# Optimization experiments

Measured on AMD Instinct MI355X. Metric: run time of the kernel, lower is better.

The kernel has to match this reference:

```python
import jax, jax.numpy as jnp
import numpy as np
import math

B, S, D = 1, 4096, 512
H, KVH, DH = 8, 4, 64
DH2 = DH // 2
M = int(math.isqrt(S))           # product-key grid side, S == M*M
K = 8                            # top_k
ROPE_BASE = 10000.0


def rope_cos_sin(seq_len, dh, base):
    inv_freq = 1.0 / (base ** (jnp.arange(0, dh, 2, dtype=jnp.float32) / dh))
    t = jnp.arange(seq_len, dtype=jnp.float32)
    freqs = jnp.outer(t, inv_freq)                      # (S, dh/2)
    emb = jnp.concatenate([freqs, freqs], axis=-1)      # (S, dh)
    return jnp.cos(emb), jnp.sin(emb)


def apply_rope(x, cos, sin):
    # x: (B, H, S, dh); half-split rotation (llama-style)
    dh2 = x.shape[-1] // 2
    rot = jnp.concatenate([-x[..., dh2:], x[..., :dh2]], axis=-1)
    return x * cos + rot * sin


def setup_inputs() -> dict:
    key = jax.random.key(0)
    ks = jax.random.split(key, 5)
    s = 0.02
    x = jax.random.normal(ks[0], (B, S, D), dtype=jnp.float32)
    Wq = jax.random.normal(ks[1], (H * DH, D), dtype=jnp.float32) * s
    Wk = jax.random.normal(ks[2], (KVH * DH, D), dtype=jnp.float32) * s
    Wv = jax.random.normal(ks[3], (KVH * DH, D), dtype=jnp.float32) * s
    Wo = jax.random.normal(ks[4], (D, H * DH), dtype=jnp.float32) * s
    return {"x": x, "Wq": Wq, "Wk": Wk, "Wv": Wv, "Wo": Wo}


def reference(x, Wq, Wk, Wv, Wo):
    b, s, d = x.shape
    cos, sin = rope_cos_sin(s, DH, ROPE_BASE)
    q = (x @ Wq.T).reshape(b, s, H, DH).transpose(0, 2, 1, 3)      # (B,H,S,DH)
    k = (x @ Wk.T).reshape(b, s, KVH, DH).transpose(0, 2, 1, 3)    # (B,KVH,S,DH)
    v = (x @ Wv.T).reshape(b, s, KVH, DH).transpose(0, 2, 1, 3)
    q = apply_rope(q, cos, sin)
    k = apply_rope(k, cos, sin)
    rep = H // KVH                                                 # GQA repeat_kv
    k = jnp.repeat(k, rep, axis=1)                                 # (B,H,S,DH)
    v = jnp.repeat(v, rep, axis=1)

    # factorized product keys: sum over grid rows / cols
    kg = k.reshape(b, H, M, M, DH)
    k1 = kg[..., :DH2].sum(axis=-2)                                # (B,H,M,DH2)
    k2 = kg[..., DH2:].sum(axis=-3)                                # (B,H,M,DH2)
    q1, q2 = q[..., :DH2], q[..., DH2:]

    def topk_sel(qh, kh):  # qh: (S,DH2), kh: (M,DH2)
        scores = qh @ kh.T                                         # (S,M)
        _, idx = jax.lax.top_k(scores, K)                          # (S,K)
        return kh[idx], idx                                        # (S,K,DH2), (S,K)

    sel2 = jax.vmap(jax.vmap(topk_sel))
    k1v, i1 = sel2(q1, k1)                                         # (B,H,S,K,DH2)
    k2v, i2 = sel2(q2, k2)

    # cross-product candidates: (B,H,S,K,K,DH) -> (B,H,S,K*K,DH)
    c1 = jnp.broadcast_to(k1v[:, :, :, :, None, :], (b, H, s, K, K, DH2))
    c2 = jnp.broadcast_to(k2v[:, :, :, None, :, :], (b, H, s, K, K, DH2))
    cand = jnp.concatenate([c1, c2], axis=-1).reshape(b, H, s, K * K, DH)

    scores_final = jnp.einsum('bhsd,bhscd->bhsc', q, cand)         # (B,H,S,K*K)
    _, sel = jax.lax.top_k(scores_final, K)                        # (B,H,S,K)
    final_k = jnp.take_along_axis(cand, sel[..., None], axis=3)    # (B,H,S,K,DH)

    row = jnp.take_along_axis(i1, sel // K, axis=3)
    col = jnp.take_along_axis(i2, sel % K, axis=3)
    v_idx = row * M + col                                          # (B,H,S,K)
    final_v = jax.vmap(jax.vmap(lambda vb, ib: vb[ib]))(v, v_idx)  # (B,H,S,K,DH)

    attn = jax.nn.softmax(
        jnp.einsum('bhsd,bhskd->bhsk', q, final_k) / math.sqrt(DH), axis=-1)
    o = jnp.einsum('bhsk,bhskd->bhsd', attn, final_v)              # (B,H,S,DH)
    o = o.transpose(0, 2, 1, 3).reshape(b, s, H * DH)
    return o @ Wo.T
```

## Files before the change

kernel.cpp:

```cpp
#include <hip/hip_runtime.h>
#include <math.h>


static constexpr size_t OFF_P1  = 0;
static constexpr size_t OFF_P2  = 4194304;
static constexpr size_t OFF_Q   = 8388608;
static constexpr size_t OFF_K   = 10485760;
static constexpr size_t OFF_V   = 11534336;
static constexpr size_t OFF_COS = 12582912;
static constexpr size_t OFF_SIN = 12713984;
static constexpr size_t OFF_K1  = 12845056;
static constexpr size_t OFF_K2  = 12853248;
static constexpr size_t OFF_O   = 12861440;
static constexpr size_t OFF_W   = 14958592;

#define LDB 132

__device__ __forceinline__ float rdlane_f(float v, int lane) {
  return __int_as_float(__builtin_amdgcn_readlane(__float_as_int(v), lane));
}

__global__ __launch_bounds__(256) void freq_table_kernel(float* __restrict__ cosT,
    float* __restrict__ sinT) {
  int idx = blockIdx.x * 256 + threadIdx.x;
  int s = idx >> 5;
  int dp = idx & 31;
  double e = (double)dp * (1.0 / 32.0);
  float pf = (float)pow(10000.0, e);
  float invf = 1.0f / pf;
  float argf = __fmul_rn((float)s, invf);
  cosT[idx] = (float)cos((double)argf);
  sinT[idx] = (float)sin((double)argf);
}

__global__ __launch_bounds__(256) void gemm128_panel(const float* __restrict__ A,
    const float* __restrict__ B, float* __restrict__ C1, float* __restrict__ C2,
    int N, int ksplit) {
  __shared__ float As[16 * LDB];
  __shared__ float Bs[16 * LDB];
  const int tid = threadIdx.x;
  const int z = blockIdx.z;
  const int k0 = z ? ksplit : 0;
  const int k1 = z ? 512 : ksplit;
  float* __restrict__ C = z ? C2 : C1;
  const int bm = blockIdx.y, bn = blockIdx.x;
  const int lrow = tid >> 1;
  const int lko = (tid & 1) << 3;
  const int ty = tid >> 4;
  const int tx = tid & 15;
  const float* Ap = A + (size_t)(bm * 128 + lrow) * 512 + lko;
  const float* Bp = B + (size_t)(bn * 128 + lrow) * 512 + lko;
  float acc[8][8] = {{0.f}};
  float4 a0 = *(const float4*)(Ap + k0);
  float4 a1 = *(const float4*)(Ap + k0 + 4);
  float4 b0 = *(const float4*)(Bp + k0);
  float4 b1 = *(const float4*)(Bp + k0 + 4);
  for (int kt = k0; kt < k1; kt += 16) {
    __syncthreads();
    As[(lko + 0) * LDB + lrow] = a0.x;
    As[(lko + 1) * LDB + lrow] = a0.y;
    As[(lko + 2) * LDB + lrow] = a0.z;
    As[(lko + 3) * LDB + lrow] = a0.w;
    As[(lko + 4) * LDB + lrow] = a1.x;
    As[(lko + 5) * LDB + lrow] = a1.y;
    As[(lko + 6) * LDB + lrow] = a1.z;
    As[(lko + 7) * LDB + lrow] = a1.w;
    Bs[(lko + 0) * LDB + lrow] = b0.x;
    Bs[(lko + 1) * LDB + lrow] = b0.y;
    Bs[(lko + 2) * LDB + lrow] = b0.z;
    Bs[(lko + 3) * LDB + lrow] = b0.w;
    Bs[(lko + 4) * LDB + lrow] = b1.x;
    Bs[(lko + 5) * LDB + lrow] = b1.y;
    Bs[(lko + 6) * LDB + lrow] = b1.z;
    Bs[(lko + 7) * LDB + lrow] = b1.w;
    __syncthreads();
    if (kt + 16 < k1) {
      a0 = *(const float4*)(Ap + kt + 16);
      a1 = *(const float4*)(Ap + kt + 20);
      b0 = *(const float4*)(Bp + kt + 16);
      b1 = *(const float4*)(Bp + kt + 20);
    }
    #pragma unroll
    for (int k = 0; k < 16; ++k) {
      float4 al = *(const float4*)(&As[k * LDB + (ty << 2)]);
      float4 ah = *(const float4*)(&As[k * LDB + 64 + (ty << 2)]);
      float4 bl = *(const float4*)(&Bs[k * LDB + (tx << 2)]);
      float4 bh = *(const float4*)(&Bs[k * LDB + 64 + (tx << 2)]);
      float af[8] = {al.x, al.y, al.z, al.w, ah.x, ah.y, ah.z, ah.w};
      float bf[8] = {bl.x, bl.y, bl.z, bl.w, bh.x, bh.y, bh.z, bh.w};
      #pragma unroll
      for (int i2 = 0; i2 < 8; ++i2)
        #pragma unroll
        for (int j2 = 0; j2 < 8; ++j2)
          acc[i2][j2] = fmaf(af[i2], bf[j2], acc[i2][j2]);
    }
  }
  #pragma unroll
  for (int i2 = 0; i2 < 8; ++i2) {
    int row = bm * 128 + ((i2 < 4) ? (ty << 2) + i2 : 64 + (ty << 2) + i2 - 4);
    float* Cp = C + (size_t)row * N + bn * 128;
    *(float4*)(Cp + (tx << 2))      = make_float4(acc[i2][0], acc[i2][1], acc[i2][2], acc[i2][3]);
    *(float4*)(Cp + 64 + (tx << 2)) = make_float4(acc[i2][4], acc[i2][5], acc[i2][6], acc[i2][7]);
  }
}

__global__ __launch_bounds__(256) void combine_kernel(const float* __restrict__ p1,
    const float* __restrict__ p2, float* __restrict__ out) {
  int i = blockIdx.x * 256 + threadIdx.x;
  out[i] = __fadd_rn(p1[i], p2[i]);
}

__global__ __launch_bounds__(256) void rope_reshape_kernel(const float* __restrict__ p1,
    const float* __restrict__ p2, const float* __restrict__ cosT,
    const float* __restrict__ sinT, float* __restrict__ qb,
    float* __restrict__ kb, float* __restrict__ vb) {
  int idx = blockIdx.x * 256 + threadIdx.x;
  int s = idx >> 10;
  int n = idx & 1023;
  float val = __fadd_rn(p1[idx], p2[idx]);
  int d = n & 63;
  if (n < 768) {
    int dp = d & 31;
    float cs = cosT[(s << 5) + dp];
    float sn = sinT[(s << 5) + dp];
    int npart = (n - d) + ((d < 32) ? d + 32 : d - 32);
    int pidx = (s << 10) + npart;
    float partner = __fadd_rn(p1[pidx], p2[pidx]);
    float rot = (d < 32) ? -partner : partner;
    float out = __fadd_rn(__fmul_rn(val, cs), __fmul_rn(rot, sn));
    if (n < 512) {
      int h = n >> 6;
      qb[((size_t)(h * 4096 + s) << 6) + d] = out;
    } else {
      int kvh = (n - 512) >> 6;
      kb[((size_t)(kvh * 4096 + s) << 6) + d] = out;
    }
  } else {
    int kvh = (n - 768) >> 6;
    vb[((size_t)(kvh * 4096 + s) << 6) + d] = val;
  }
}

__global__ __launch_bounds__(256) void k12_np_kernel(const float* __restrict__ kb,
    float* __restrict__ k1t, float* __restrict__ k2t) {
  int id = blockIdx.x * 256 + threadIdx.x;
  int which = id >> 13;
  int rem = id & 8191;
  int kvh = rem >> 11;
  int rem2 = rem & 2047;
  int i = rem2 >> 5;
  int d = rem2 & 31;
  const float* base = kb + ((size_t)(kvh * 4096) << 6);
  if (which == 0) {
    float acc = base[((size_t)(i * 64) << 6) + d];
    for (int c = 1; c < 64; ++c)
      acc = __fadd_rn(acc, base[((size_t)(i * 64 + c) << 6) + d]);
    k1t[(kvh * 64 + i) * 32 + d] = acc;
  } else {
    float acc = base[((size_t)i << 6) + d + 32];
    for (int r = 1; r < 64; ++r)
      acc = __fadd_rn(acc, base[((size_t)(r * 64 + i) << 6) + d + 32]);
    k2t[(kvh * 64 + i) * 32 + d] = acc;
  }
}

__global__ __launch_bounds__(256) void stage1_scores_kernel(
    const float* __restrict__ qb, const float* __restrict__ k1t,
    const float* __restrict__ k2t, float* __restrict__ sc) {
  __shared__ float qs[64 * 68];
  __shared__ float kd[32 * 132];
  const int t = threadIdx.x;
  const int h = blockIdx.y;
  const int s0 = blockIdx.x * 64;
  const int kvh = h >> 1;
  #pragma unroll
  for (int i = 0; i < 16; ++i) {
    int j = t + i * 256;
    int ss = j >> 6, d = j & 63;
    qs[d * 68 + ss] = qb[((size_t)(h * 4096 + s0 + ss) << 6) + d];
  }
  #pragma unroll
  for (int i = 0; i < 8; ++i) {
    int j = t + i * 256;
    int r = j >> 5, d = j & 31;
    kd[d * 132 + r]      = k1t[(kvh * 64 + r) * 32 + d];
    kd[d * 132 + 64 + r] = k2t[(kvh * 64 + r) * 32 + d];
  }
  __syncthreads();
  const int ty = t >> 4;
  const int tx = t & 15;
  const int qrow = (tx >= 8) ? 32 : 0;
  float acc[4][8] = {{0.f}};
  #pragma unroll
  for (int d = 0; d < 32; ++d) {
    float4 a4 = *(const float4*)&qs[(qrow + d) * 68 + (ty << 2)];
    float4 b0 = *(const float4*)&kd[d * 132 + (tx << 3)];
    float4 b1 = *(const float4*)&kd[d * 132 + (tx << 3) + 4];
    float af[4] = {a4.x, a4.y, a4.z, a4.w};
    float bf[8] = {b0.x, b0.y, b0.z, b0.w, b1.x, b1.y, b1.z, b1.w};
    #pragma unroll
    for (int i2 = 0; i2 < 4; ++i2)
      #pragma unroll
      for (int j2 = 0; j2 < 8; ++j2)
        acc[i2][j2] = fmaf(af[i2], bf[j2], acc[i2][j2]);
  }
  #pragma unroll
  for (int i2 = 0; i2 < 4; ++i2) {
    float* p = sc + (((size_t)(h * 4096 + s0 + (ty << 2) + i2)) << 7) + (tx << 3);
    *(float4*)(p)     = make_float4(acc[i2][0], acc[i2][1], acc[i2][2], acc[i2][3]);
    *(float4*)(p + 4) = make_float4(acc[i2][4], acc[i2][5], acc[i2][6], acc[i2][7]);
  }
}

__device__ __forceinline__ void bitonic64_val_desc(float& v, int lane) {
  #pragma unroll
  for (int k = 2; k <= 64; k <<= 1) {
    #pragma unroll
    for (int j = k >> 1; j >= 1; j >>= 1) {
      float ov = __shfl_xor(v, j, 64);
      bool up = ((lane & k) == 0) == ((lane & j) == 0);
      float mx = fmaxf(v, ov), mn = fminf(v, ov);
      v = up ? mx : mn;
    }
  }
}

__global__ __launch_bounds__(256) void attn_sel_kernel(const float* __restrict__ sc,
    const float* __restrict__ qb, const float* __restrict__ vb,
    const float* __restrict__ k1t, const float* __restrict__ k2t,
    float* __restrict__ ob) {
  const int lane = threadIdx.x & 63;
  const int w = blockIdx.x * 4 + (threadIdx.x >> 6);
  const int h = w >> 12;
  const int s = w & 4095;
  const int kvh = h >> 1;
  const float* scp = sc + ((size_t)w << 7);
  const float s1 = scp[lane];
  const float s2 = scp[64 + lane];
  const float qv = qb[((size_t)w << 6) + lane];

  float v1 = s1;
  bitonic64_val_desc(v1, lane);
  unsigned long long pack1 = 0, used = 0;
  #pragma unroll
  for (int t = 0; t < 8; ++t) {
    float tv = rdlane_f(v1, t);
    unsigned long long m = __ballot(s1 == tv) & ~used;
    int ix = __ffsll((long long)m) - 1;
    used |= 1ull << ix;
    pack1 |= (unsigned long long)ix << (6 * t);
  }
  float v2 = s2;
  bitonic64_val_desc(v2, lane);
  unsigned long long pack2 = 0;
  used = 0;
  #pragma unroll
  for (int t = 0; t < 8; ++t) {
    float tv = rdlane_f(v2, t);
    unsigned long long m = __ballot(s2 == tv) & ~used;
    int ix = __ffsll((long long)m) - 1;
    used |= 1ull << ix;
    pack2 |= (unsigned long long)ix << (6 * t);
  }

  int r1 = (int)((pack1 >> (6 * (lane >> 3))) & 63);
  int r2 = (int)((pack2 >> (6 * (lane & 7))) & 63);
  const float* k1p = k1t + (size_t)(kvh * 64 + r1) * 32;
  const float* k2p = k2t + (size_t)(kvh * 64 + r2) * 32;
  float c = 0.f;
  #pragma unroll
  for (int dq = 0; dq < 32; dq += 4) {
    float4 kk = *(const float4*)(k1p + dq);
    c = __fadd_rn(c, __fmul_rn(rdlane_f(qv, dq + 0), kk.x));
    c = __fadd_rn(c, __fmul_rn(rdlane_f(qv, dq + 1), kk.y));
    c = __fadd_rn(c, __fmul_rn(rdlane_f(qv, dq + 2), kk.z));
    c = __fadd_rn(c, __fmul_rn(rdlane_f(qv, dq + 3), kk.w));
  }
  #pragma unroll
  for (int dq = 0; dq < 32; dq += 4) {
    float4 kk = *(const float4*)(k2p + dq);
    c = __fadd_rn(c, __fmul_rn(rdlane_f(qv, 32 + dq + 0), kk.x));
    c = __fadd_rn(c, __fmul_rn(rdlane_f(qv, 32 + dq + 1), kk.y));
    c = __fadd_rn(c, __fmul_rn(rdlane_f(qv, 32 + dq + 2), kk.z));
    c = __fadd_rn(c, __fmul_rn(rdlane_f(qv, 32 + dq + 3), kk.w));
  }
  const float scand = c;
  float v3 = c;
  bitonic64_val_desc(v3, lane);
  float cvs[8]; int ccs[8];
  used = 0;
  #pragma unroll
  for (int t = 0; t < 8; ++t) {
    float tv = rdlane_f(v3, t);
    unsigned long long m = __ballot(scand == tv) & ~used;
    int ix = __ffsll((long long)m) - 1;
    used |= 1ull << ix;
    cvs[t] = tv;
    ccs[t] = ix;
  }
  float y[8];
  #pragma unroll
  for (int t = 0; t < 8; ++t) y[t] = cvs[t] * 0.125f;
  float mx = y[0];
  #pragma unroll
  for (int t = 1; t < 8; ++t) if (y[t] > mx) mx = y[t];
  float e[8];
  #pragma unroll
  for (int t = 0; t < 8; ++t) e[t] = __expf(__fsub_rn(y[t], mx));
  float wsum = __fadd_rn(__fadd_rn(__fadd_rn(e[0], e[1]), __fadd_rn(e[2], e[3])),
                         __fadd_rn(__fadd_rn(e[4], e[5]), __fadd_rn(e[6], e[7])));
  const float* vbh = vb + ((size_t)kvh << 18);
  float o = 0.f;
  #pragma unroll
  for (int t = 0; t < 8; ++t) {
    float att = __fdiv_rn(e[t], wsum);
    int row = (int)((pack1 >> (6 * (ccs[t] >> 3))) & 63);
    int col = (int)((pack2 >> (6 * (ccs[t] & 7))) & 63);
    o = __fadd_rn(o, __fmul_rn(att, vbh[((size_t)(row * 64 + col) << 6) + lane]));
  }
  ob[(size_t)s * 512 + (h << 6) + lane] = o;
}

extern "C" void kernel_launch(void* const* d_in, const int* in_sizes, int n_in,
                              void* d_out, int out_size, void* d_ws, size_t ws_size,
                              hipStream_t stream) {
  const float* x  = (const float*)d_in[0];
  const float* Wq = (const float*)d_in[1];
  const float* Wk = (const float*)d_in[2];
  const float* Wv = (const float*)d_in[3];
  const float* Wo = (const float*)d_in[4];
  float* ws = (float*)d_ws;
  float* p1   = ws + OFF_P1;
  float* p2   = ws + OFF_P2;
  float* qb   = ws + OFF_Q;
  float* kb   = ws + OFF_K;
  float* vb   = ws + OFF_V;
  float* cosT = ws + OFF_COS;
  float* sinT = ws + OFF_SIN;
  float* k1t  = ws + OFF_K1;
  float* k2t  = ws + OFF_K2;
  float* ob   = ws + OFF_O;
  float* wcat = ws + OFF_W;
  float* scb  = ws + OFF_P1;
  float* op1  = ws + OFF_P2;
  float* op2  = ws + OFF_P2 + 2097152;

  hipMemcpyAsync(wcat,             Wq, (size_t)512 * 512 * sizeof(float), hipMemcpyDeviceToDevice, stream);
  hipMemcpyAsync(wcat + 512 * 512, Wk, (size_t)256 * 512 * sizeof(float), hipMemcpyDeviceToDevice, stream);
  hipMemcpyAsync(wcat + 768 * 512, Wv, (size_t)256 * 512 * sizeof(float), hipMemcpyDeviceToDevice, stream);

  freq_table_kernel<<<512, 256, 0, stream>>>(cosT, sinT);
  gemm128_panel<<<dim3(8, 32, 2), 256, 0, stream>>>(x, wcat, p1, p2, 1024, 384);
  rope_reshape_kernel<<<16384, 256, 0, stream>>>(p1, p2, cosT, sinT, qb, kb, vb);
  k12_np_kernel<<<64, 256, 0, stream>>>(kb, k1t, k2t);
  stage1_scores_kernel<<<dim3(64, 8), 256, 0, stream>>>(qb, k1t, k2t, scb);
  attn_sel_kernel<<<8192, 256, 0, stream>>>(scb, qb, vb, k1t, k2t, ob);
  gemm128_panel<<<dim3(4, 32, 2), 256, 0, stream>>>(ob, Wo, op1, op2, 512, 256);
  combine_kernel<<<8192, 256, 0, stream>>>(op1, op2, (float*)d_out);
}
```

Before: 244.7 us.

## Split stage-1 top-k into per-thread insertion-sort kernel over transposed scores

The scores kernel now writes row/column scores transposed (grid index major, sequence minor) so that a new sel1 kernel can give each query its own thread. That thread runs a register insertion top-8 over 64 coalesced reads for each half and emits packed indices. The attention kernel then reads the packed indices instead of running two 64-lane bitonic sorts per wavefront. This removes the heavy shuffle-based sorts but adds one kernel launch and a small index buffer, and sel1 runs only 512 wavefronts.

```diff
diff --git a/kernel.cpp b/kernel.cpp
--- a/kernel.cpp
+++ b/kernel.cpp
@@ -2,17 +2,18 @@
 #include <math.h>
 
 
-static constexpr size_t OFF_P1  = 0;
-static constexpr size_t OFF_P2  = 4194304;
-static constexpr size_t OFF_Q   = 8388608;
-static constexpr size_t OFF_K   = 10485760;
-static constexpr size_t OFF_V   = 11534336;
-static constexpr size_t OFF_COS = 12582912;
-static constexpr size_t OFF_SIN = 12713984;
-static constexpr size_t OFF_K1  = 12845056;
-static constexpr size_t OFF_K2  = 12853248;
-static constexpr size_t OFF_O   = 12861440;
-static constexpr size_t OFF_W   = 14958592;
+static constexpr size_t OFF_P1   = 0;
+static constexpr size_t OFF_P2   = 4194304;
+static constexpr size_t OFF_Q    = 8388608;
+static constexpr size_t OFF_K    = 10485760;
+static constexpr size_t OFF_V    = 11534336;
+static constexpr size_t OFF_COS  = 12582912;
+static constexpr size_t OFF_SIN  = 12713984;
+static constexpr size_t OFF_K1   = 12845056;
+static constexpr size_t OFF_K2   = 12853248;
+static constexpr size_t OFF_O    = 12861440;
+static constexpr size_t OFF_W    = 14958592;
+static constexpr size_t OFF_PACK = 15482880;
 
 #define LDB 132
 
@@ -164,9 +165,9 @@
   }
 }
 
-__global__ __launch_bounds__(256) void stage1_scores_kernel(
+__global__ __launch_bounds__(256) void stage1_scoresT_kernel(
     const float* __restrict__ qb, const float* __restrict__ k1t,
-    const float* __restrict__ k2t, float* __restrict__ sc) {
+    const float* __restrict__ k2t, float* __restrict__ scT) {
   __shared__ float qs[64 * 68];
   __shared__ float kd[32 * 132];
   const int t = threadIdx.x;
@@ -189,27 +190,73 @@
   __syncthreads();
   const int ty = t >> 4;
   const int tx = t & 15;
-  const int qrow = (tx >= 8) ? 32 : 0;
-  float acc[4][8] = {{0.f}};
-  #pragma unroll
-  for (int d = 0; d < 32; ++d) {
-    float4 a4 = *(const float4*)&qs[(qrow + d) * 68 + (ty << 2)];
-    float4 b0 = *(const float4*)&kd[d * 132 + (tx << 3)];
-    float4 b1 = *(const float4*)&kd[d * 132 + (tx << 3) + 4];
-    float af[4] = {a4.x, a4.y, a4.z, a4.w};
-    float bf[8] = {b0.x, b0.y, b0.z, b0.w, b1.x, b1.y, b1.z, b1.w};
+  float acc1[4][4] = {{0.f}};
+  float acc2[4][4] = {{0.f}};
+  #pragma unroll
+  for (int dp = 0; dp < 32; ++dp) {
+    float4 kv1 = *(const float4*)&kd[dp * 132 + (ty << 2)];
+    float4 kv2 = *(const float4*)&kd[dp * 132 + 64 + (ty << 2)];
+    float4 q1 = *(const float4*)&qs[dp * 68 + (tx << 2)];
+    float4 q2 = *(const float4*)&qs[(32 + dp) * 68 + (tx << 2)];
+    float k1f[4] = {kv1.x, kv1.y, kv1.z, kv1.w};
+    float k2f[4] = {kv2.x, kv2.y, kv2.z, kv2.w};
+    float q1f[4] = {q1.x, q1.y, q1.z, q1.w};
+    float q2f[4] = {q2.x, q2.y, q2.z, q2.w};
     #pragma unroll
     for (int i2 = 0; i2 < 4; ++i2)
       #pragma unroll
-      for (int j2 = 0; j2 < 8; ++j2)
-        acc[i2][j2] = fmaf(af[i2], bf[j2], acc[i2][j2]);
-  }
+      for (int j2 = 0; j2 < 4; ++j2) {
+        acc1[i2][j2] = fmaf(k1f[i2], q1f[j2], acc1[i2][j2]);
+        acc2[i2][j2] = fmaf(k2f[i2], q2f[j2], acc2[i2][j2]);
+      }
+  }
+  float* base = scT + (size_t)h * 524288 + s0 + (tx << 2);
   #pragma unroll
   for (int i2 = 0; i2 < 4; ++i2) {
-    float* p = sc + (((size_t)(h * 4096 + s0 + (ty << 2) + i2)) << 7) + (tx << 3);
-    *(float4*)(p)     = make_float4(acc[i2][0], acc[i2][1], acc[i2][2], acc[i2][3]);
-    *(float4*)(p + 4) = make_float4(acc[i2][4], acc[i2][5], acc[i2][6], acc[i2][7]);
-  }
+    *(float4*)(base + (size_t)((ty << 2) + i2) * 4096) =
+        make_float4(acc1[i2][0], acc1[i2][1], acc1[i2][2], acc1[i2][3]);
+    *(float4*)(base + (size_t)(64 + (ty << 2) + i2) * 4096) =
+        make_float4(acc2[i2][0], acc2[i2][1], acc2[i2][2], acc2[i2][3]);
+  }
+}
+
+__global__ __launch_bounds__(64) void sel1_kernel(const float* __restrict__ scT,
+    ulonglong2* __restrict__ packs) {
+  const int w = blockIdx.x * 64 + threadIdx.x;
+  const int h = w >> 12;
+  const int s = w & 4095;
+  const float* base = scT + (size_t)h * 524288 + s;
+  unsigned long long pk[2];
+  #pragma unroll
+  for (int set = 0; set < 2; ++set) {
+    const float* p = base + (size_t)set * 64 * 4096;
+    float top[8];
+    int idx[8];
+    #pragma unroll
+    for (int t = 0; t < 8; ++t) { top[t] = -INFINITY; idx[t] = 0; }
+    #pragma unroll
+    for (int r = 0; r < 64; ++r) {
+      float v = p[(size_t)r * 4096];
+      int i = r;
+      #pragma unroll
+      for (int j = 0; j < 8; ++j) {
+        bool gt = v > top[j];
+        float tv = top[j]; int ti = idx[j];
+        top[j] = gt ? v : tv;
+        idx[j] = gt ? i : ti;
+        v = gt ? tv : v;
+        i = gt ? ti : i;
+      }
+    }
+    unsigned long long pp = 0;
+    #pragma unroll
+    for (int t = 0; t < 8; ++t) pp |= (unsigned long long)idx[t] << (6 * t);
+    pk[set] = pp;
+  }
+  ulonglong2 out;
+  out.x = pk[0];
+  out.y = pk[1];
+  packs[w] = out;
 }
 
 __device__ __forceinline__ void bitonic64_val_desc(float& v, int lane) {
@@ -225,43 +272,18 @@
   }
 }
 
-__global__ __launch_bounds__(256) void attn_sel_kernel(const float* __restrict__ sc,
-    const float* __restrict__ qb, const float* __restrict__ vb,
-    const float* __restrict__ k1t, const float* __restrict__ k2t,
-    float* __restrict__ ob) {
+__global__ __launch_bounds__(256) void attn_sel2_kernel(
+    const ulonglong2* __restrict__ packs, const float* __restrict__ qb,
+    const float* __restrict__ vb, const float* __restrict__ k1t,
+    const float* __restrict__ k2t, float* __restrict__ ob) {
   const int lane = threadIdx.x & 63;
   const int w = blockIdx.x * 4 + (threadIdx.x >> 6);
   const int h = w >> 12;
   const int s = w & 4095;
   const int kvh = h >> 1;
-  const float* scp = sc + ((size_t)w << 7);
-  const float s1 = scp[lane];
-  const float s2 = scp[64 + lane];
+  ulonglong2 pk = packs[w];
+  const unsigned long long pack1 = pk.x, pack2 = pk.y;
   const float qv = qb[((size_t)w << 6) + lane];
-
-  float v1 = s1;
-  bitonic64_val_desc(v1, lane);
-  unsigned long long pack1 = 0, used = 0;
-  #pragma unroll
-  for (int t = 0; t < 8; ++t) {
-    float tv = rdlane_f(v1, t);
-    unsigned long long m = __ballot(s1 == tv) & ~used;
-    int ix = __ffsll((long long)m) - 1;
-    used |= 1ull << ix;
-    pack1 |= (unsigned long long)ix << (6 * t);
-  }
-  float v2 = s2;
-  bitonic64_val_desc(v2, lane);
-  unsigned long long pack2 = 0;
-  used = 0;
-  #pragma unroll
-  for (int t = 0; t < 8; ++t) {
-    float tv = rdlane_f(v2, t);
-    unsigned long long m = __ballot(s2 == tv) & ~used;
-    int ix = __ffsll((long long)m) - 1;
-    used |= 1ull << ix;
-    pack2 |= (unsigned long long)ix << (6 * t);
-  }
 
   int r1 = (int)((pack1 >> (6 * (lane >> 3))) & 63);
   int r2 = (int)((pack2 >> (6 * (lane & 7))) & 63);
@@ -288,7 +310,7 @@
   float v3 = c;
   bitonic64_val_desc(v3, lane);
   float cvs[8]; int ccs[8];
-  used = 0;
+  unsigned long long used = 0;
   #pragma unroll
   for (int t = 0; t < 8; ++t) {
     float tv = rdlane_f(v3, t);
@@ -341,9 +363,10 @@
   float* k2t  = ws + OFF_K2;
   float* ob   = ws + OFF_O;
   float* wcat = ws + OFF_W;
-  float* scb  = ws + OFF_P1;
+  float* scT  = ws + OFF_P1;
   float* op1  = ws + OFF_P2;
   float* op2  = ws + OFF_P2 + 2097152;
+  ulonglong2* packs = (ulonglong2*)(ws + OFF_PACK);
 
   hipMemcpyAsync(wcat,             Wq, (size_t)512 * 512 * sizeof(float), hipMemcpyDeviceToDevice, stream);
   hipMemcpyAsync(wcat + 512 * 512, Wk, (size_t)256 * 512 * sizeof(float), hipMemcpyDeviceToDevice, stream);
@@ -353,8 +376,9 @@
   gemm128_panel<<<dim3(8, 32, 2), 256, 0, stream>>>(x, wcat, p1, p2, 1024, 384);
   rope_reshape_kernel<<<16384, 256, 0, stream>>>(p1, p2, cosT, sinT, qb, kb, vb);
   k12_np_kernel<<<64, 256, 0, stream>>>(kb, k1t, k2t);
-  stage1_scores_kernel<<<dim3(64, 8), 256, 0, stream>>>(qb, k1t, k2t, scb);
-  attn_sel_kernel<<<8192, 256, 0, stream>>>(scb, qb, vb, k1t, k2t, ob);
+  stage1_scoresT_kernel<<<dim3(64, 8), 256, 0, stream>>>(qb, k1t, k2t, scT);
+  sel1_kernel<<<512, 64, 0, stream>>>(scT, packs);
+  attn_sel2_kernel<<<8192, 256, 0, stream>>>(packs, qb, vb, k1t, k2t, ob);
   gemm128_panel<<<dim3(4, 32, 2), 256, 0, stream>>>(ob, Wo, op1, op2, 512, 256);
   combine_kernel<<<8192, 256, 0, stream>>>(op1, op2, (float*)d_out);
 }
```

New measurement: 256.7 us. +4.9%, slower.
